# Optimization experiments

Hardware: AMD Instinct MI355X
Metric: run time of the kernel (lower is better)

The kernel has to match this reference:

```python
import jax, jax.numpy as jnp
import numpy as np

B, C, H, W = 1, 256, 64, 64
K_DIM, V_DIM, HEADS = 64, 64, 8


def setup_inputs() -> dict:
    key = jax.random.key(0)
    ks = jax.random.split(key, 13)
    s = lambda i, shape: jax.random.normal(ks[i], shape, dtype=jnp.float32) * 0.05
    return {
        "x": s(0, (B, C, H, W)),
        # low-rank bottleneck projections (bias=False), torch Linear weight is [out,in]
        "wq1": s(1, (K_DIM // 2, C)),
        "wk1": s(2, (K_DIM // 2, C)),
        "wv1": s(3, (V_DIM // 2, C)),
        # expansion to per-head dims (bias=False)
        "wq2": s(4, (K_DIM * HEADS, K_DIM // 2)),
        "wk2": s(5, (K_DIM * HEADS, K_DIM // 2)),
        "wv2": s(6, (V_DIM * HEADS, V_DIM // 2)),
        # output projection (with bias)
        "wo": s(7, (C, V_DIM * HEADS)),
        "bo": s(8, (C,)),
        # depthwise 3x3 conv (groups=C): [C,1,3,3]
        "w_dw": s(9, (C, 1, 3, 3)),
        "b_dw": s(10, (C,)),
        # 1x1 gate conv
        "w_gate": s(11, (C, C, 1, 1)),
        "b_gate": s(12, (C,)),
    }


def reference(x, wq1, wk1, wv1, wq2, wk2, wv2, wo, bo, w_dw, b_dw, w_gate, b_gate):
    B_, C_, H_, W_ = x.shape
    N = H_ * W_
    t = x.transpose(0, 2, 3, 1).reshape(B_, N, C_)  # [B, N, C]
    # low-rank then expansion: Linear(x) = x @ W.T
    q = (t @ wq1.T) @ wq2.T  # [B, N, HEADS*K_DIM]
    k = (t @ wk1.T) @ wk2.T
    v = (t @ wv1.T) @ wv2.T
    q = q.reshape(B_, N, HEADS, K_DIM).transpose(0, 2, 1, 3)  # [B,h,N,dk]
    k = k.reshape(B_, N, HEADS, K_DIM).transpose(0, 2, 1, 3)
    v = v.reshape(B_, N, HEADS, V_DIM).transpose(0, 2, 1, 3)
    attn = jnp.einsum('bhnd,bhmd->bhnm', q, k) / jnp.sqrt(jnp.float32(K_DIM))
    attn = jax.nn.softmax(attn, axis=-1)
    out = jnp.einsum('bhnm,bhmd->bhnd', attn, v)  # [B,h,N,dv]
    out = out.transpose(0, 2, 1, 3).reshape(B_, N, HEADS * V_DIM)
    out = out @ wo.T + bo  # [B, N, C]
    out = out.reshape(B_, H_, W_, C_).transpose(0, 3, 1, 2)  # NCHW
    dn = ('NCHW', 'OIHW', 'NCHW')
    out = jax.lax.conv_general_dilated(out, w_dw, (1, 1), 'SAME', dimension_numbers=dn,
                                       feature_group_count=C_) + b_dw[None, :, None, None]
    gate = jax.nn.sigmoid(
        jax.lax.conv_general_dilated(out, w_gate, (1, 1), 'SAME', dimension_numbers=dn)
        + b_gate[None, :, None, None])
    return out * gate
```

## Files before the change

kernel.cpp:

```cpp
#include <hip/hip_runtime.h>

typedef __bf16 bf16;
typedef __bf16 bf16x4 __attribute__((ext_vector_type(4)));
typedef __bf16 bf16x8 __attribute__((ext_vector_type(8)));
typedef float f32x4 __attribute__((ext_vector_type(4)));

#define MFMA16(a, b, c) __builtin_amdgcn_mfma_f32_16x16x32_bf16((a), (b), (c), 0, 0, 0)

__device__ inline float fexp2(float x) {
    float r;
    asm("v_exp_f32 %0, %1" : "=v"(r) : "v"(x));
    return r;
}

__global__ void k_pre(const float* __restrict__ x, bf16* __restrict__ xt,
                      const float* __restrict__ wq1, const float* __restrict__ wk1,
                      const float* __restrict__ wv1, const float* __restrict__ wq2,
                      const float* __restrict__ wk2, const float* __restrict__ wv2,
                      const float* __restrict__ wo, const float* __restrict__ wg,
                      bf16* __restrict__ Wq, bf16* __restrict__ Wk, bf16* __restrict__ Wv,
                      bf16* __restrict__ wo_bf, bf16* __restrict__ wg_bf) {
    __shared__ float tile[64][68];
    const int bx = blockIdx.x;
    if (bx < 256) {
        const int t = threadIdx.x;
        const int c0 = (bx & 3) * 64;
        const int n0 = (bx >> 2) * 64;
        {
            const int cr = t >> 4, nc = (t & 15) * 4;
#pragma unroll
            for (int i = 0; i < 4; ++i) {
                const float4 v = *(const float4*)(x + (size_t)(c0 + cr + i * 16) * 4096 + n0 + nc);
                tile[cr + i * 16][nc + 0] = v.x;
                tile[cr + i * 16][nc + 1] = v.y;
                tile[cr + i * 16][nc + 2] = v.z;
                tile[cr + i * 16][nc + 3] = v.w;
            }
        }
        __syncthreads();
        const int n = t >> 2, cc = (t & 3) * 16;
        bf16x8 o0, o1;
#pragma unroll
        for (int j = 0; j < 8; ++j) o0[j] = (bf16)tile[cc + j][n];
#pragma unroll
        for (int j = 0; j < 8; ++j) o1[j] = (bf16)tile[cc + 8 + j][n];
        bf16* dst = xt + (size_t)(n0 + n) * 256 + c0 + cc;
        *(bf16x8*)dst = o0;
        *(bf16x8*)(dst + 8) = o1;
    } else {
        int t = (bx - 256) * 256 + threadIdx.x;
        if (t < 393216) {
            int which = t >> 17;
            int rem = t & 131071;
            int o = rem >> 8, c = rem & 255;
            const float* w1 = which == 0 ? wq1 : which == 1 ? wk1 : wv1;
            const float* w2 = which == 0 ? wq2 : which == 1 ? wk2 : wv2;
            float acc = 0.f;
#pragma unroll
            for (int j = 0; j < 32; ++j) acc += w2[o * 32 + j] * w1[j * 256 + c];
            bf16* W = which == 0 ? Wq : which == 1 ? Wk : Wv;
            W[o * 256 + c] = (bf16)acc;
        } else if (t < 524288) {
            int idx = t - 393216;
            wo_bf[idx] = (bf16)wo[idx];
        } else if (t < 589824) {
            int idx = t - 524288;
            wg_bf[idx] = (bf16)wg[idx];
        }
    }
}

template <int MODE>
__device__ __forceinline__ void gemm_body(const bf16* __restrict__ A, const bf16* __restrict__ B,
                                          int K, float scale, void* __restrict__ outp,
                                          const float* __restrict__ bias,
                                          const float* __restrict__ mul, int bx, int by) {
    const int lane = threadIdx.x & 63;
    const int w = threadIdx.x >> 6;
    const int i0 = by * 128 + w * 32;
    const int j0 = bx * 64;
    const int lrow = lane & 15;
    const int lk = (lane >> 4) * 8;

    f32x4 acc[2][4];
#pragma unroll
    for (int a = 0; a < 2; ++a)
#pragma unroll
        for (int b = 0; b < 4; ++b) acc[a][b] = (f32x4){0.f, 0.f, 0.f, 0.f};

    for (int k0 = 0; k0 < K; k0 += 32) {
        bf16x8 af[2], bfr[4];
#pragma unroll
        for (int qs = 0; qs < 2; ++qs)
            af[qs] = *(const bf16x8*)(A + (size_t)(i0 + qs * 16 + lrow) * K + k0 + lk);
#pragma unroll
        for (int js = 0; js < 4; ++js)
            bfr[js] = *(const bf16x8*)(B + (size_t)(j0 + js * 16 + lrow) * K + k0 + lk);
#pragma unroll
        for (int qs = 0; qs < 2; ++qs)
#pragma unroll
            for (int js = 0; js < 4; ++js)
                acc[qs][js] = MFMA16(af[qs], bfr[js], acc[qs][js]);
    }

    const int rbase = (lane >> 4) * 4;
#pragma unroll
    for (int qs = 0; qs < 2; ++qs)
#pragma unroll
        for (int js = 0; js < 4; ++js)
#pragma unroll
            for (int r = 0; r < 4; ++r) {
                int i = i0 + qs * 16 + rbase + r;
                int j = j0 + js * 16 + lrow;
                float v = acc[qs][js][r];
                if (MODE == 0) {
                    ((bf16*)outp)[(size_t)(j >> 6) * (4096 * 64) + (size_t)i * 64 + (j & 63)] =
                        (bf16)(v * scale);
                } else if (MODE == 1) {
                    ((bf16*)outp)[(size_t)i * 4096 + j] = (bf16)v;
                } else if (MODE == 2) {
                    ((float*)outp)[(size_t)i * 4096 + j] = v + bias[i];
                } else {
                    float g = v + bias[i];
                    float sg = 1.f / (1.f + __expf(-g));
                    ((float*)outp)[(size_t)i * 4096 + j] = mul[(size_t)i * 4096 + j] * sg;
                }
            }
}

template <int MODE>
__launch_bounds__(256)
__global__ void k_gemm_nt(const bf16* __restrict__ A, const bf16* __restrict__ B,
                          int K, float scale, void* __restrict__ outp,
                          const float* __restrict__ bias, const float* __restrict__ mul) {
    gemm_body<MODE>(A, B, K, scale, outp, bias, mul, blockIdx.x, blockIdx.y);
}

__launch_bounds__(256)
__global__ void k_qkv(const bf16* __restrict__ xbf, const bf16* __restrict__ Wq,
                      const bf16* __restrict__ Wk, const bf16* __restrict__ Wv,
                      bf16* __restrict__ q_buf, bf16* __restrict__ k_buf,
                      bf16* __restrict__ vT, float qscale) {
    const int b = blockIdx.x;
    if (b < 256) {
        gemm_body<0>(xbf, Wq, 256, qscale, q_buf, nullptr, nullptr, b & 7, b >> 3);
    } else if (b < 512) {
        const int bb = b - 256;
        gemm_body<0>(xbf, Wk, 256, 1.0f, k_buf, nullptr, nullptr, bb & 7, bb >> 3);
    } else {
        const int bb = b - 512;
        gemm_body<1>(Wv, xbf, 256, 1.0f, vT, nullptr, nullptr, bb & 63, bb >> 6);
    }
}

__launch_bounds__(256)
__global__ void k_attn(const bf16* __restrict__ q, const bf16* __restrict__ k,
                       const bf16* __restrict__ vT, bf16* __restrict__ Opart,
                       float* __restrict__ lpart) {
    __shared__ char kvlds[16384];
    __shared__ char plds[4][4096];
    const int tid = threadIdx.x;
    const int lane = tid & 63;
    const int w = tid >> 6;
    const int split = blockIdx.x >> 8;
    const int h = (blockIdx.x >> 5) & 7;
    const int qt = blockIdx.x & 31;
    const int qbase = qt * 128 + w * 32;
    const int lrow = lane & 15;
    const int g = lane >> 4;
    const int swzr = (lrow & 7) << 4;

    const bf16* qh = q + (size_t)h * 4096 * 64;
    const bf16* kh = k + (size_t)h * 4096 * 64;
    const bf16* vh = vT + (size_t)h * 64 * 4096;
    char* myp = plds[w];
    const char* Kl = kvlds;
    const char* Vl = kvlds + 8192;

    const int isV = tid >> 7;
    const int srow = (tid & 127) >> 1;
    const int shalf = tid & 1;
    const int swzs = (srow & 7) << 4;
    char* ldst = kvlds + isV * 8192 + srow * 128;
    const bf16* sbase = isV ? (vh + (size_t)srow * 4096 + split * 1024 + shalf * 32)
                            : (kh + ((size_t)split * 1024 + srow) * 64 + shalf * 32);
    const size_t sstep = isV ? 64 : 64 * 64;

    bf16x8 bq[2][2];
#pragma unroll
    for (int qs = 0; qs < 2; ++qs)
#pragma unroll
        for (int ks = 0; ks < 2; ++ks)
            bq[qs][ks] = *(const bf16x8*)(qh + (size_t)(qbase + qs * 16 + lrow) * 64 +
                                          ks * 32 + g * 8);

    f32x4 accO[2][4];
    f32x4 l_acc[2];
#pragma unroll
    for (int qs = 0; qs < 2; ++qs) {
#pragma unroll
        for (int ds = 0; ds < 4; ++ds) accO[qs][ds] = (f32x4){0.f, 0.f, 0.f, 0.f};
        l_acc[qs] = (f32x4){0.f, 0.f, 0.f, 0.f};
    }
    bf16x8 ones;
#pragma unroll
    for (int i = 0; i < 8; ++i) ones[i] = (bf16)1.0f;

    uint4 r0, r1, r2, r3;
    {
        const bf16* p = sbase;
        r0 = *(const uint4*)(p);
        r1 = *(const uint4*)(p + 8);
        r2 = *(const uint4*)(p + 16);
        r3 = *(const uint4*)(p + 24);
    }

    for (int t = 0; t < 16; ++t) {
        *(uint4*)(ldst + ((shalf * 64 + 0) ^ swzs)) = r0;
        *(uint4*)(ldst + ((shalf * 64 + 16) ^ swzs)) = r1;
        *(uint4*)(ldst + ((shalf * 64 + 32) ^ swzs)) = r2;
        *(uint4*)(ldst + ((shalf * 64 + 48) ^ swzs)) = r3;
        if (t < 15) {
            const bf16* p = sbase + (size_t)(t + 1) * sstep;
            r0 = *(const uint4*)(p);
            r1 = *(const uint4*)(p + 8);
            r2 = *(const uint4*)(p + 16);
            r3 = *(const uint4*)(p + 24);
        }
        __syncthreads();

#pragma unroll
        for (int qs = 0; qs < 2; ++qs) {
            const int qrow = qs * 16 + lrow;
            f32x4 s[4];
#pragma unroll
            for (int js = 0; js < 4; ++js) s[js] = (f32x4){0.f, 0.f, 0.f, 0.f};
            __builtin_amdgcn_s_setprio(1);
#pragma unroll
            for (int ks = 0; ks < 2; ++ks) {
                bf16x8 ak[4];
#pragma unroll
                for (int js = 0; js < 4; ++js)
                    ak[js] = *(const bf16x8*)(Kl + (js * 16 + lrow) * 128 +
                                              ((ks * 64 + g * 16) ^ swzr));
#pragma unroll
                for (int js = 0; js < 4; ++js)
                    s[js] = MFMA16(ak[js], bq[qs][ks], s[js]);
            }
            __builtin_amdgcn_s_setprio(0);
#pragma unroll
            for (int js = 0; js < 4; ++js) {
                bf16x4 pk;
#pragma unroll
                for (int r = 0; r < 4; ++r) pk[r] = (bf16)fexp2(s[js][r]);
                *(bf16x4*)(myp + ((qrow * 128 + js * 32 + g * 8) ^ swzr)) = pk;
            }
            __builtin_amdgcn_s_setprio(1);
#pragma unroll
            for (int ks2 = 0; ks2 < 2; ++ks2) {
                bf16x8 ap = *(const bf16x8*)(myp + ((qrow * 128 + ks2 * 64 + g * 16) ^ swzr));
                bf16x8 bv[4];
#pragma unroll
                for (int ds = 0; ds < 4; ++ds)
                    bv[ds] = *(const bf16x8*)(Vl + (ds * 16 + lrow) * 128 +
                                              ((ks2 * 64 + g * 16) ^ swzr));
#pragma unroll
                for (int ds = 0; ds < 4; ++ds)
                    accO[qs][ds] = MFMA16(ap, bv[ds], accO[qs][ds]);
                l_acc[qs] = MFMA16(ap, ones, l_acc[qs]);
            }
            __builtin_amdgcn_s_setprio(0);
        }
        __syncthreads();
    }

#pragma unroll
    for (int qs = 0; qs < 2; ++qs)
#pragma unroll
        for (int ds = 0; ds < 4; ++ds)
#pragma unroll
            for (int r = 0; r < 4; ++r) {
                const int n = qbase + qs * 16 + 4 * g + r;
                Opart[((size_t)split * 4096 + n) * 512 + h * 64 + ds * 16 + lrow] =
                    (bf16)accO[qs][ds][r];
            }
    if (lrow == 0) {
#pragma unroll
        for (int qs = 0; qs < 2; ++qs)
#pragma unroll
            for (int r = 0; r < 4; ++r)
                lpart[((size_t)split * 8 + h) * 4096 + qbase + qs * 16 + 4 * g + r] =
                    l_acc[qs][r];
    }
}

__global__ void k_combine(const bf16* __restrict__ Opart, const float* __restrict__ lpart,
                          bf16* __restrict__ o) {
    const int tid = blockIdx.x * 256 + threadIdx.x;
    const int n = tid >> 6;
    const int c8 = (tid & 63) * 8;
    const int h = c8 >> 6;
    float acc[8] = {0, 0, 0, 0, 0, 0, 0, 0};
    float l = 0.f;
#pragma unroll
    for (int s = 0; s < 4; ++s) {
        const bf16x8 v = *(const bf16x8*)(Opart + ((size_t)s * 4096 + n) * 512 + c8);
#pragma unroll
        for (int j = 0; j < 8; ++j) acc[j] += (float)v[j];
        l += lpart[((size_t)s * 8 + h) * 4096 + n];
    }
    const float inv = 1.f / l;
    bf16x8 ov;
#pragma unroll
    for (int j = 0; j < 8; ++j) ov[j] = (bf16)(acc[j] * inv);
    *(bf16x8*)(o + (size_t)n * 512 + c8) = ov;
}

__global__ void k_dw(const float* __restrict__ y, const float* __restrict__ wdw,
                     const float* __restrict__ bdw, float* __restrict__ dwout,
                     bf16* __restrict__ dwt) {
    int t = blockIdx.x * 256 + threadIdx.x;
    int c = t >> 12, n = t & 4095, yy = n >> 6, xx = n & 63;
    float acc = bdw[c];
    const float* yc = y + (size_t)c * 4096;
#pragma unroll
    for (int ky = 0; ky < 3; ++ky) {
        int ry = yy + ky - 1;
        if ((unsigned)ry < 64u) {
#pragma unroll
            for (int kx = 0; kx < 3; ++kx) {
                int rx = xx + kx - 1;
                if ((unsigned)rx < 64u) acc += wdw[c * 9 + ky * 3 + kx] * yc[ry * 64 + rx];
            }
        }
    }
    dwout[t] = acc;
    dwt[n * 256 + c] = (bf16)acc;
}

extern "C" void kernel_launch(void* const* d_in, const int* in_sizes, int n_in,
                              void* d_out, int out_size, void* d_ws, size_t ws_size,
                              hipStream_t stream) {
    const float* x   = (const float*)d_in[0];
    const float* wq1 = (const float*)d_in[1];
    const float* wk1 = (const float*)d_in[2];
    const float* wv1 = (const float*)d_in[3];
    const float* wq2 = (const float*)d_in[4];
    const float* wk2 = (const float*)d_in[5];
    const float* wv2 = (const float*)d_in[6];
    const float* wo  = (const float*)d_in[7];
    const float* bo  = (const float*)d_in[8];
    const float* wdw = (const float*)d_in[9];
    const float* bdw = (const float*)d_in[10];
    const float* wg  = (const float*)d_in[11];
    const float* bg  = (const float*)d_in[12];

    char* ws = (char*)d_ws;
    size_t off = 0;
    auto alloc = [&](size_t bytes) {
        char* p = ws + off;
        off += (bytes + 255) & ~(size_t)255;
        return p;
    };
    bf16*  q_buf = (bf16*)alloc((size_t)8 * 4096 * 64 * 2);
    bf16*  k_buf = (bf16*)alloc((size_t)8 * 4096 * 64 * 2);
    bf16*  vT    = (bf16*)alloc((size_t)8 * 64 * 4096 * 2);
    bf16*  o_buf = (bf16*)alloc((size_t)4096 * 512 * 2);
    bf16*  wo_bf = (bf16*)alloc((size_t)256 * 512 * 2);
    bf16*  wg_bf = (bf16*)alloc((size_t)256 * 256 * 2);
    char* U = ws + off;
    bf16*  xbf = (bf16*)U;
    bf16*  Wq  = (bf16*)(U + (size_t)2 * 1024 * 1024);
    bf16*  Wk  = (bf16*)(U + (size_t)2 * 1024 * 1024 + 262144);
    bf16*  Wv  = (bf16*)(U + (size_t)2 * 1024 * 1024 + 524288);
    bf16*  Opart = (bf16*)U;
    float* lpart = (float*)(U + (size_t)16 * 1024 * 1024);
    float* ybuf  = (float*)U;
    float* dwout = (float*)(U + (size_t)4 * 1024 * 1024);
    bf16*  dwt   = (bf16*)(U + (size_t)8 * 1024 * 1024);
    (void)ws_size; (void)in_sizes; (void)n_in; (void)out_size;

    const float QSCALE = 0.125f * 1.4426950408889634f;

    k_pre<<<2560, 256, 0, stream>>>(x, xbf, wq1, wk1, wv1, wq2, wk2, wv2, wo, wg,
                                    Wq, Wk, Wv, wo_bf, wg_bf);
    k_qkv<<<768, 256, 0, stream>>>(xbf, Wq, Wk, Wv, q_buf, k_buf, vT, QSCALE);
    k_attn<<<1024, 256, 0, stream>>>(q_buf, k_buf, vT, Opart, lpart);
    k_combine<<<1024, 256, 0, stream>>>(Opart, lpart, o_buf);
    k_gemm_nt<2><<<dim3(64, 2), 256, 0, stream>>>(wo_bf, o_buf, 512, 1.0f, ybuf, bo, nullptr);
    k_dw<<<4096, 256, 0, stream>>>(ybuf, wdw, bdw, dwout, dwt);
    k_gemm_nt<3><<<dim3(64, 2), 256, 0, stream>>>(wg_bf, dwt, 256, 1.0f, d_out, bg, dwout);
}
```

Measured before the change: 121.6 us.

## Split output GEMMs into smaller tiles and batch attention MFMAs across query subtiles

The output-projection and gate GEMMs get a new kernel with 64x64 tiles (16 rows per wave), which doubles the grid from 128 to 256 blocks so more of the CUs have work. In the attention loop, the QK^T MFMAs for both 16-row query subtiles are now issued together, and in the PV step each V fragment is loaded once and reused for both subtiles. This raises instruction-level parallelism and removes duplicate LDS reads of K and V, at the cost of more live registers for the score tiles. The smaller GEMM tiles lower per-wave reuse of the B operand.

```diff
diff --git a/kernel.cpp b/kernel.cpp
--- a/kernel.cpp
+++ b/kernel.cpp
@@ -73,8 +73,7 @@
 template <int MODE>
 __device__ __forceinline__ void gemm_body(const bf16* __restrict__ A, const bf16* __restrict__ B,
                                           int K, float scale, void* __restrict__ outp,
-                                          const float* __restrict__ bias,
-                                          const float* __restrict__ mul, int bx, int by) {
+                                          int bx, int by) {
     const int lane = threadIdx.x & 63;
     const int w = threadIdx.x >> 6;
     const int i0 = by * 128 + w * 32;
@@ -116,24 +115,55 @@
                 if (MODE == 0) {
                     ((bf16*)outp)[(size_t)(j >> 6) * (4096 * 64) + (size_t)i * 64 + (j & 63)] =
                         (bf16)(v * scale);
-                } else if (MODE == 1) {
+                } else {
                     ((bf16*)outp)[(size_t)i * 4096 + j] = (bf16)v;
-                } else if (MODE == 2) {
-                    ((float*)outp)[(size_t)i * 4096 + j] = v + bias[i];
-                } else {
-                    float g = v + bias[i];
-                    float sg = 1.f / (1.f + __expf(-g));
-                    ((float*)outp)[(size_t)i * 4096 + j] = mul[(size_t)i * 4096 + j] * sg;
                 }
             }
 }
 
 template <int MODE>
 __launch_bounds__(256)
-__global__ void k_gemm_nt(const bf16* __restrict__ A, const bf16* __restrict__ B,
-                          int K, float scale, void* __restrict__ outp,
-                          const float* __restrict__ bias, const float* __restrict__ mul) {
-    gemm_body<MODE>(A, B, K, scale, outp, bias, mul, blockIdx.x, blockIdx.y);
+__global__ void k_gemm64(const bf16* __restrict__ A, const bf16* __restrict__ B,
+                         int K, void* __restrict__ outp,
+                         const float* __restrict__ bias, const float* __restrict__ mul) {
+    const int lane = threadIdx.x & 63;
+    const int w = threadIdx.x >> 6;
+    const int i0 = blockIdx.y * 64 + w * 16;
+    const int j0 = blockIdx.x * 64;
+    const int lrow = lane & 15;
+    const int lk = (lane >> 4) * 8;
+
+    f32x4 acc[4];
+#pragma unroll
+    for (int b = 0; b < 4; ++b) acc[b] = (f32x4){0.f, 0.f, 0.f, 0.f};
+
+    for (int k0 = 0; k0 < K; k0 += 32) {
+        bf16x8 af = *(const bf16x8*)(A + (size_t)(i0 + lrow) * K + k0 + lk);
+        bf16x8 bfr[4];
+#pragma unroll
+        for (int js = 0; js < 4; ++js)
+            bfr[js] = *(const bf16x8*)(B + (size_t)(j0 + js * 16 + lrow) * K + k0 + lk);
+#pragma unroll
+        for (int js = 0; js < 4; ++js)
+            acc[js] = MFMA16(af, bfr[js], acc[js]);
+    }
+
+    const int rbase = (lane >> 4) * 4;
+#pragma unroll
+    for (int js = 0; js < 4; ++js)
+#pragma unroll
+        for (int r = 0; r < 4; ++r) {
+            int i = i0 + rbase + r;
+            int j = j0 + js * 16 + lrow;
+            float v = acc[js][r];
+            if (MODE == 2) {
+                ((float*)outp)[(size_t)i * 4096 + j] = v + bias[i];
+            } else {
+                float g2 = v + bias[i];
+                float sg = 1.f / (1.f + __expf(-g2));
+                ((float*)outp)[(size_t)i * 4096 + j] = mul[(size_t)i * 4096 + j] * sg;
+            }
+        }
 }
 
 __launch_bounds__(256)
@@ -143,13 +173,13 @@
                       bf16* __restrict__ vT, float qscale) {
     const int b = blockIdx.x;
     if (b < 256) {
-        gemm_body<0>(xbf, Wq, 256, qscale, q_buf, nullptr, nullptr, b & 7, b >> 3);
+        gemm_body<0>(xbf, Wq, 256, qscale, q_buf, b & 7, b >> 3);
     } else if (b < 512) {
         const int bb = b - 256;
-        gemm_body<0>(xbf, Wk, 256, 1.0f, k_buf, nullptr, nullptr, bb & 7, bb >> 3);
+        gemm_body<0>(xbf, Wk, 256, 1.0f, k_buf, bb & 7, bb >> 3);
     } else {
         const int bb = b - 512;
-        gemm_body<1>(Wv, xbf, 256, 1.0f, vT, nullptr, nullptr, bb & 63, bb >> 6);
+        gemm_body<1>(Wv, xbf, 256, 1.0f, vT, bb & 63, bb >> 6);
     }
 }
 
@@ -229,48 +259,59 @@
         }
         __syncthreads();
 
+        f32x4 s[2][4];
+#pragma unroll
+        for (int qs = 0; qs < 2; ++qs)
+#pragma unroll
+            for (int js = 0; js < 4; ++js) s[qs][js] = (f32x4){0.f, 0.f, 0.f, 0.f};
+        __builtin_amdgcn_s_setprio(1);
+#pragma unroll
+        for (int ks = 0; ks < 2; ++ks) {
+            bf16x8 ak[4];
+#pragma unroll
+            for (int js = 0; js < 4; ++js)
+                ak[js] = *(const bf16x8*)(Kl + (js * 16 + lrow) * 128 +
+                                          ((ks * 64 + g * 16) ^ swzr));
+#pragma unroll
+            for (int qs = 0; qs < 2; ++qs)
+#pragma unroll
+                for (int js = 0; js < 4; ++js)
+                    s[qs][js] = MFMA16(ak[js], bq[qs][ks], s[qs][js]);
+        }
+        __builtin_amdgcn_s_setprio(0);
+
 #pragma unroll
         for (int qs = 0; qs < 2; ++qs) {
             const int qrow = qs * 16 + lrow;
-            f32x4 s[4];
-#pragma unroll
-            for (int js = 0; js < 4; ++js) s[js] = (f32x4){0.f, 0.f, 0.f, 0.f};
-            __builtin_amdgcn_s_setprio(1);
-#pragma unroll
-            for (int ks = 0; ks < 2; ++ks) {
-                bf16x8 ak[4];
-#pragma unroll
-                for (int js = 0; js < 4; ++js)
-                    ak[js] = *(const bf16x8*)(Kl + (js * 16 + lrow) * 128 +
-                                              ((ks * 64 + g * 16) ^ swzr));
-#pragma unroll
-                for (int js = 0; js < 4; ++js)
-                    s[js] = MFMA16(ak[js], bq[qs][ks], s[js]);
-            }
-            __builtin_amdgcn_s_setprio(0);
 #pragma unroll
             for (int js = 0; js < 4; ++js) {
                 bf16x4 pk;
 #pragma unroll
-                for (int r = 0; r < 4; ++r) pk[r] = (bf16)fexp2(s[js][r]);
+                for (int r = 0; r < 4; ++r) pk[r] = (bf16)fexp2(s[qs][js][r]);
                 *(bf16x4*)(myp + ((qrow * 128 + js * 32 + g * 8) ^ swzr)) = pk;
             }
-            __builtin_amdgcn_s_setprio(1);
-#pragma unroll
-            for (int ks2 = 0; ks2 < 2; ++ks2) {
-                bf16x8 ap = *(const bf16x8*)(myp + ((qrow * 128 + ks2 * 64 + g * 16) ^ swzr));
-                bf16x8 bv[4];
-#pragma unroll
-                for (int ds = 0; ds < 4; ++ds)
-                    bv[ds] = *(const bf16x8*)(Vl + (ds * 16 + lrow) * 128 +
-                                              ((ks2 * 64 + g * 16) ^ swzr));
-#pragma unroll
-                for (int ds = 0; ds < 4; ++ds)
-                    accO[qs][ds] = MFMA16(ap, bv[ds], accO[qs][ds]);
-                l_acc[qs] = MFMA16(ap, ones, l_acc[qs]);
-            }
-            __builtin_amdgcn_s_setprio(0);
-        }
+        }
+
+        __builtin_amdgcn_s_setprio(1);
+#pragma unroll
+        for (int ks2 = 0; ks2 < 2; ++ks2) {
+            bf16x8 bv[4];
+#pragma unroll
+            for (int ds = 0; ds < 4; ++ds)
+                bv[ds] = *(const bf16x8*)(Vl + (ds * 16 + lrow) * 128 +
+                                          ((ks2 * 64 + g * 16) ^ swzr));
+            bf16x8 ap0 = *(const bf16x8*)(myp + ((lrow * 128 + ks2 * 64 + g * 16) ^ swzr));
+            bf16x8 ap1 = *(const bf16x8*)(myp + (((16 + lrow) * 128 + ks2 * 64 + g * 16) ^ swzr));
+#pragma unroll
+            for (int ds = 0; ds < 4; ++ds)
+                accO[0][ds] = MFMA16(ap0, bv[ds], accO[0][ds]);
+            l_acc[0] = MFMA16(ap0, ones, l_acc[0]);
+#pragma unroll
+            for (int ds = 0; ds < 4; ++ds)
+                accO[1][ds] = MFMA16(ap1, bv[ds], accO[1][ds]);
+            l_acc[1] = MFMA16(ap1, ones, l_acc[1]);
+        }
+        __builtin_amdgcn_s_setprio(0);
         __syncthreads();
     }
 
@@ -387,7 +428,7 @@
     k_qkv<<<768, 256, 0, stream>>>(xbf, Wq, Wk, Wv, q_buf, k_buf, vT, QSCALE);
     k_attn<<<1024, 256, 0, stream>>>(q_buf, k_buf, vT, Opart, lpart);
     k_combine<<<1024, 256, 0, stream>>>(Opart, lpart, o_buf);
-    k_gemm_nt<2><<<dim3(64, 2), 256, 0, stream>>>(wo_bf, o_buf, 512, 1.0f, ybuf, bo, nullptr);
+    k_gemm64<2><<<dim3(64, 4), 256, 0, stream>>>(wo_bf, o_buf, 512, ybuf, bo, nullptr);
     k_dw<<<4096, 256, 0, stream>>>(ybuf, wdw, bdw, dwout, dwt);
-    k_gemm_nt<3><<<dim3(64, 2), 256, 0, stream>>>(wg_bf, dwt, 256, 1.0f, d_out, bg, dwout);
-}
+    k_gemm64<3><<<dim3(64, 4), 256, 0, stream>>>(wg_bf, dwt, 256, d_out, bg, dwout);
+}
```

After: 114.6 us. 5.8% less time.
